# Kernel optimization log

Hardware: AMD Instinct MI355X
Metric: run time of the kernel (lower is better)

The kernel has to match this reference:

```python
import jax, jax.numpy as jnp
import numpy as np

N = 50000      # nodes
E = 800000     # edges (avg degree 16)
DIN = 128      # input_dim
DH = 128       # hidden_dim
H = 8          # num_heads
DK = DH // H   # 16
TN = 8         # num_node_types
TE = 8         # num_edge_types
NB = 4         # num_bases


def setup_inputs() -> dict:
    key = jax.random.key(0)
    ks = jax.random.split(key, 20)
    inp = {}
    inp['node_feat'] = jax.random.normal(ks[0], (N, DIN), jnp.float32)
    inp['node_type'] = jax.random.randint(ks[1], (N,), 0, TN)
    inp['src'] = jax.random.randint(ks[2], (E,), 0, N)
    inp['dst'] = jax.random.randint(ks[3], (E,), 0, N)
    inp['edge_type'] = jax.random.randint(ks[4], (E,), 0, TE)
    s = 0.05
    for i, nm in enumerate(['k', 'q', 'v', 'a']):
        inp['w_comp_' + nm] = jax.random.normal(ks[5 + 2 * i], (TN, NB), jnp.float32) * s
        inp['w_basis_' + nm] = jax.random.normal(ks[6 + 2 * i], (NB, DIN * DH), jnp.float32) * s
    inp['relation_pri'] = jnp.ones((TE, H), jnp.float32)
    inp['relation_att'] = jax.random.uniform(ks[13], (TE, H, DK, DK), jnp.float32, -0.25, 0.25)
    inp['relation_msg'] = jax.random.uniform(ks[14], (TE, H, DK, DK), jnp.float32, -0.25, 0.25)
    inp['loop_weight'] = jax.random.uniform(ks[15], (DIN, DH), jnp.float32, -0.08, 0.08)
    inp['bias'] = jnp.zeros((DH,), jnp.float32)
    return inp


def _decomp(x, nt, w_comp, w_basis):
    # basis regularizer: per-node-type weight W[t] = sum_b w_comp[t,b] * basis[b]
    T = w_comp.shape[0]
    W = (w_comp @ w_basis).reshape(T, x.shape[-1], -1)   # [T, in, out]
    h_all = jnp.einsum('ni,tio->tno', x, W)              # [T, N, out]
    return h_all[nt, jnp.arange(x.shape[0])]             # gather per-node type


def reference(node_feat, node_type, src, dst, edge_type,
              w_comp_k, w_basis_k, w_comp_q, w_basis_q,
              w_comp_v, w_basis_v, w_comp_a, w_basis_a,
              relation_pri, relation_att, relation_msg, loop_weight, bias):
    n = node_feat.shape[0]
    scale = (DH / H) ** -0.5
    # node init: k/q/v projections (per-node-type basis transforms)
    k = _decomp(node_feat, node_type, w_comp_k, w_basis_k).reshape(n, H, DK)
    q = _decomp(node_feat, node_type, w_comp_q, w_basis_q).reshape(n, H, DK)
    v = _decomp(node_feat, node_type, w_comp_v, w_basis_v).reshape(n, H, DK)
    # edge init: HGT attention. kt = k[src] @ relation_att[etype], computed
    # per-type at node granularity then gathered (avoids [E,H,dk,dk] gather).
    kt = jnp.einsum('nhi,thij->tnhj', k, relation_att)[edge_type, src]   # [E,H,dk]
    e = (q[dst] * kt).sum(-1) * relation_pri[edge_type] * scale          # [E,H]
    # edge softmax over incoming edges of each dst node
    m = jax.ops.segment_max(e, dst, num_segments=n)
    ex = jnp.exp(e - m[dst])
    denom = jax.ops.segment_sum(ex, dst, num_segments=n)
    a = ex / denom[dst]                                                  # [E,H]
    # message: v[src] @ relation_msg[etype], weighted by attention, sum-reduce
    vt = jnp.einsum('nhi,thij->tnhj', v, relation_msg)[edge_type, src]   # [E,H,dk]
    agg = jax.ops.segment_sum(a[..., None] * vt, dst, num_segments=n)    # [N,H,dk]
    agg = agg.reshape(n, DH)
    # node update: a_transform + self loop + bias + relu (dropout=0, no BN)
    out = _decomp(agg, node_type, w_comp_a, w_basis_a)
    out = out + node_feat @ loop_weight + bias
    return jax.nn.relu(out)
```

## Files before the change

### kernel.cpp

```cpp
#include <hip/hip_runtime.h>
#include <hip/hip_bf16.h>
#include <stdint.h>

#define DIN 128
#define DHID 128
#define NHEAD 8
#define DKH 16
#define TN 8
#define TE 8
#define NBASE 4

typedef short s8v __attribute__((ext_vector_type(8)));
typedef float f4v __attribute__((ext_vector_type(4)));

static __device__ __forceinline__ float bf2f(__hip_bfloat16 x){ return __bfloat162float(x); }
static __device__ __forceinline__ float lo16f(uint32_t u){ return __builtin_bit_cast(float, u << 16); }
static __device__ __forceinline__ float hi16f(uint32_t u){ return __builtin_bit_cast(float, u & 0xFFFF0000u); }
static __device__ __forceinline__ uint16_t f2bfu(float x){ return __builtin_bit_cast(uint16_t, __float2bfloat16(x)); }
static __device__ __forceinline__ uint32_t packbf2(float lo, float hi){
    return (uint32_t)f2bfu(lo) | ((uint32_t)f2bfu(hi) << 16);
}
static __device__ __forceinline__ float ldf(const void* p, int i, int flag){
    return flag ? ((const float*)p)[i] : bf2f(((const __hip_bfloat16*)p)[i]);
}

__global__ void k_hist(const int* __restrict__ dst, int E,
                       const int* __restrict__ ntype, int Nn,
                       int* __restrict__ deg, int* __restrict__ tcount,
                       const uint32_t* __restrict__ rpri_raw, int* __restrict__ dflag)
{
    __shared__ int lt[TN];
    if (threadIdx.x < TN) lt[threadIdx.x] = 0;
    if (blockIdx.x == 0 && threadIdx.x == 0) {
        dflag[0] = (rpri_raw[0] == 0x3F803F80u) ? 0 : 1;
    }
    __syncthreads();
    int stride = gridDim.x * blockDim.x;
    int i0 = blockIdx.x * blockDim.x + threadIdx.x;
    for (int e = i0; e < E; e += stride) atomicAdd(&deg[dst[e]], 1);
    for (int n = i0; n < Nn; n += stride) atomicAdd(&lt[ntype[n]], 1);
    __syncthreads();
    if (threadIdx.x < TN) atomicAdd(&tcount[threadIdx.x], lt[threadIdx.x]);
}

__global__ void k_convert(const void* __restrict__ xin, uint32_t* __restrict__ xbf,
                          int nWords, const int* __restrict__ dflag)
{
    int flag = dflag[0];
    int i = blockIdx.x * 256 + threadIdx.x;
    int stride = gridDim.x * 256;
    if (flag) {
        const float2* f = (const float2*)xin;
        for (int w = i; w < nWords; w += stride) {
            float2 v = f[w];
            xbf[w] = packbf2(v.x, v.y);
        }
    } else {
        const uint32_t* s = (const uint32_t*)xin;
        for (int w = i; w < nWords; w += stride) xbf[w] = s[w];
    }
}

__global__ void k_weights(const void* __restrict__ ck, const void* __restrict__ bk,
                          const void* __restrict__ cq, const void* __restrict__ bq,
                          const void* __restrict__ cv, const void* __restrict__ bv,
                          const void* __restrict__ ca, const void* __restrict__ ba,
                          const void* __restrict__ lw,
                          __hip_bfloat16* __restrict__ WkqvT, __hip_bfloat16* __restrict__ WfinT,
                          const int* __restrict__ dflag)
{
    int flag = dflag[0];
    int idx = blockIdx.x * 256 + threadIdx.x;
    const int T1 = TN * 3 * 128 * 128;
    if (idx < T1) {
        int t = idx / 49152; int r = idx % 49152;
        int proj = r / 16384; int r2 = r % 16384;
        int j = r2 >> 7; int i = r2 & 127;
        const void* c = (proj == 0) ? ck : ((proj == 1) ? cq : cv);
        const void* b = (proj == 0) ? bk : ((proj == 1) ? bq : bv);
        float s = 0.f;
        #pragma unroll
        for (int bb = 0; bb < NBASE; ++bb)
            s += ldf(c, t * NBASE + bb, flag) * ldf(b, bb * 16384 + i * 128 + j, flag);
        WkqvT[idx] = __float2bfloat16(s);
    } else if (idx < T1 + TN * 128 * 256) {
        int r = idx - T1;
        int t = r >> 15; int r2 = r & 32767;
        int j = r2 >> 8; int kk = r2 & 255;
        float s;
        if (kk < 128) {
            s = 0.f;
            #pragma unroll
            for (int bb = 0; bb < NBASE; ++bb)
                s += ldf(ca, t * NBASE + bb, flag) * ldf(ba, bb * 16384 + kk * 128 + j, flag);
        } else {
            s = ldf(lw, (kk - 128) * 128 + j, flag);
        }
        WfinT[r] = __float2bfloat16(s);
    }
}

__global__ void __launch_bounds__(1024) k_scan(const int* __restrict__ deg,
                                               int* __restrict__ eoff, int* __restrict__ ecur,
                                               const int* __restrict__ tcount,
                                               int* __restrict__ toff, int* __restrict__ tcur, int Nn)
{
    __shared__ int wsum[16];
    __shared__ int carry_s;
    int tid = threadIdx.x, lane = tid & 63, wid = tid >> 6;
    if (tid == 0) carry_s = 0;
    __syncthreads();
    for (int base = 0; base < Nn; base += 4096) {
        int i0 = base + tid * 4;
        int v0 = (i0     < Nn) ? deg[i0]     : 0;
        int v1 = (i0 + 1 < Nn) ? deg[i0 + 1] : 0;
        int v2 = (i0 + 2 < Nn) ? deg[i0 + 2] : 0;
        int v3 = (i0 + 3 < Nn) ? deg[i0 + 3] : 0;
        int s = v0 + v1 + v2 + v3;
        int sc = s;
        #pragma unroll
        for (int off = 1; off < 64; off <<= 1) {
            int tt = __shfl_up(sc, off, 64);
            if (lane >= off) sc += tt;
        }
        if (lane == 63) wsum[wid] = sc;
        int carry = carry_s;
        __syncthreads();
        int wb = 0;
        for (int w = 0; w < wid; ++w) wb += wsum[w];
        int run = carry + wb + (sc - s);
        if (i0     < Nn) { eoff[i0]     = run; ecur[i0]     = run; } run += v0;
        if (i0 + 1 < Nn) { eoff[i0 + 1] = run; ecur[i0 + 1] = run; } run += v1;
        if (i0 + 2 < Nn) { eoff[i0 + 2] = run; ecur[i0 + 2] = run; } run += v2;
        if (i0 + 3 < Nn) { eoff[i0 + 3] = run; ecur[i0 + 3] = run; }
        __syncthreads();
        if (tid == 0) {
            int tot = 0;
            for (int w = 0; w < 16; ++w) tot += wsum[w];
            carry_s += tot;
        }
        __syncthreads();
    }
    if (tid == 0) {
        eoff[Nn] = carry_s;
        int s = 0;
        for (int t = 0; t < TN; ++t) { toff[t] = s; tcur[t] = s; s += tcount[t]; }
        toff[TN] = s;
    }
}

__global__ void k_scatter(const int* __restrict__ src, const int* __restrict__ dst,
                          const int* __restrict__ et, int E,
                          const int* __restrict__ ntype, int Nn,
                          int* __restrict__ ecur, int* __restrict__ esrc, int* __restrict__ eet,
                          int* __restrict__ tcur, int* __restrict__ perm)
{
    int stride = gridDim.x * blockDim.x;
    int i0 = blockIdx.x * blockDim.x + threadIdx.x;
    for (int e = i0; e < E; e += stride) {
        int p = atomicAdd(&ecur[dst[e]], 1);
        esrc[p] = src[e]; eet[p] = et[e];
    }
    for (int n = i0; n < Nn; n += stride) {
        int p = atomicAdd(&tcur[ntype[n]], 1);
        perm[p] = n;
    }
}

__global__ void __launch_bounds__(256, 1) k_proj(
    const __hip_bfloat16* __restrict__ xbf,
    const __hip_bfloat16* __restrict__ WkqvT,
    const int* __restrict__ perm, const int* __restrict__ ntype,
    __hip_bfloat16* __restrict__ k16, __hip_bfloat16* __restrict__ q16,
    __hip_bfloat16* __restrict__ v16, int Nn)
{
    int lane = threadIdx.x & 63;
    int wave = blockIdx.x * 4 + (threadIdx.x >> 6);
    int row0 = wave * 16;
    if (row0 >= Nn) return;
    int col = lane & 15, quad = lane >> 4;
    int ar = row0 + col;
    int anode = perm[(ar < Nn) ? ar : (Nn - 1)];
    int tfirst = ntype[perm[row0]];
    int last_i = row0 + 15; if (last_i >= Nn) last_i = Nn - 1;
    int tlast = ntype[perm[last_i]];
    int onode[4], otype[4];
    #pragma unroll
    for (int r = 0; r < 4; ++r) {
        int oi = row0 + quad * 4 + r;
        bool v = (oi < Nn);
        onode[r] = perm[v ? oi : (Nn - 1)];
        otype[r] = v ? ntype[onode[r]] : -1;
    }
    const s8v* arow = (const s8v*)(xbf + (size_t)anode * DIN);
    for (int t = tfirst; t <= tlast; ++t) {
        f4v acc[24];
        #pragma unroll
        for (int nb = 0; nb < 24; ++nb) acc[nb] = (f4v){0.f, 0.f, 0.f, 0.f};
        const __hip_bfloat16* bbase = WkqvT + (size_t)t * 49152;
        #pragma unroll
        for (int kq = 0; kq < 4; ++kq) {
            s8v a = arow[kq * 4 + quad];
            #pragma unroll
            for (int nb = 0; nb < 24; ++nb) {
                int J = nb * 16 + col;
                s8v b = *((const s8v*)(bbase + (size_t)J * 128) + (kq * 4 + quad));
                acc[nb] = __builtin_amdgcn_mfma_f32_16x16x32_bf16(a, b, acc[nb], 0, 0, 0);
            }
        }
        #pragma unroll
        for (int nb = 0; nb < 24; ++nb) {
            int jj = ((nb * 16) & 127) + col;
            __hip_bfloat16* outp = (nb < 8) ? k16 : ((nb < 16) ? q16 : v16);
            #pragma unroll
            for (int r = 0; r < 4; ++r) {
                if (otype[r] == t) outp[(size_t)onode[r] * DHID + jj] = __float2bfloat16(acc[nb][r]);
            }
        }
    }
}

__global__ void __launch_bounds__(512, 4) k_edge(
    const __hip_bfloat16* __restrict__ k16, const __hip_bfloat16* __restrict__ q16,
    const __hip_bfloat16* __restrict__ v16,
    const void* __restrict__ ratt, const void* __restrict__ rmsg,
    const void* __restrict__ rpri,
    const int* __restrict__ eoff, const int* __restrict__ esrc, const int* __restrict__ eet,
    __hip_bfloat16* __restrict__ aggbf, int Nn, const int* __restrict__ dflag)
{
    __shared__ uint32_t Au[8192];
    __shared__ uint32_t Mu[8192];
    int flag = dflag[0];
    int tid = threadIdx.x;
    for (int d = tid; d < 4096; d += 512) {
        int et = d >> 9, ip = (d >> 6) & 7, hh = (d >> 3) & 7, xx = d & 7;
        int i0 = ip * 2, j0 = xx * 2;
        int bidx = ((et * 8 + hh) * 16 + i0) * 16 + j0;
        int o = ((et * 64 + ip * 8 + hh) * 8 + xx) * 2;
        float ps = ldf(rpri, et * 8 + hh, flag) * 0.25f;
        {
            float a00 = ldf(ratt, bidx, flag) * ps,      a10 = ldf(ratt, bidx + 16, flag) * ps;
            float a01 = ldf(ratt, bidx + 1, flag) * ps,  a11 = ldf(ratt, bidx + 17, flag) * ps;
            Au[o] = packbf2(a00, a10); Au[o + 1] = packbf2(a01, a11);
        }
        {
            float a00 = ldf(rmsg, bidx, flag),      a10 = ldf(rmsg, bidx + 16, flag);
            float a01 = ldf(rmsg, bidx + 1, flag),  a11 = ldf(rmsg, bidx + 17, flag);
            Mu[o] = packbf2(a00, a10); Mu[o + 1] = packbf2(a01, a11);
        }
    }
    __syncthreads();
    int lane = tid & 63;
    int h = lane >> 3, x = lane & 7;
    int wid = blockIdx.x * 8 + (tid >> 6);
    int nw = gridDim.x * 8;
    const uint32_t* kp = (const uint32_t*)k16;
    const uint32_t* qp = (const uint32_t*)q16;
    const uint32_t* vp = (const uint32_t*)v16;
    int lbase = h * 16 + x * 2;
    for (int n = wid; n < Nn; n += nw) {
        uint32_t qw = qp[n * 64 + lane];
        float q0 = lo16f(qw), q1 = hi16f(qw);
        float l = 0.f, a0 = 0.f, a1 = 0.f;
        int p0 = eoff[n], p1 = eoff[n + 1];
        for (int base = p0; base < p1; base += 64) {
            int myp = base + lane;
            int se = 0, te = 0;
            if (myp < p1) { se = esrc[myp]; te = eet[myp]; }
            int cnt = p1 - base; if (cnt > 64) cnt = 64;

            auto process = [&](int j) {
                int srcn = __shfl(se, j, 64);
                int et   = __shfl(te, j, 64);
                const uint4* kr = (const uint4*)(kp + (size_t)srcn * 64 + h * 8);
                uint4 ka = kr[0], kb = kr[1];
                const uint4* vr = (const uint4*)(vp + (size_t)srcn * 64 + h * 8);
                uint4 va = vr[0], vb = vr[1];
                int tb = et * 1024 + lbase;
                float u0 = 0.f, u1 = 0.f;
                {
                    uint32_t w0[8] = {ka.x, ka.y, ka.z, ka.w, kb.x, kb.y, kb.z, kb.w};
                    #pragma unroll
                    for (int ip = 0; ip < 8; ++ip) {
                        float k0 = lo16f(w0[ip]), k1 = hi16f(w0[ip]);
                        uint2 av = *(const uint2*)&Au[tb + ip * 128];
                        u0 = fmaf(k0, lo16f(av.x), u0); u0 = fmaf(k1, hi16f(av.x), u0);
                        u1 = fmaf(k0, lo16f(av.y), u1); u1 = fmaf(k1, hi16f(av.y), u1);
                    }
                }
                float pl = u0 * q0 + u1 * q1;
                pl += __shfl_xor(pl, 1, 64);
                pl += __shfl_xor(pl, 2, 64);
                pl += __shfl_xor(pl, 4, 64);
                float ex = __expf(pl);
                float t0 = 0.f, t1 = 0.f;
                {
                    uint32_t w1[8] = {va.x, va.y, va.z, va.w, vb.x, vb.y, vb.z, vb.w};
                    #pragma unroll
                    for (int ip = 0; ip < 8; ++ip) {
                        float v0 = lo16f(w1[ip]), v1 = hi16f(w1[ip]);
                        uint2 mv = *(const uint2*)&Mu[tb + ip * 128];
                        t0 = fmaf(v0, lo16f(mv.x), t0); t0 = fmaf(v1, hi16f(mv.x), t0);
                        t1 = fmaf(v0, lo16f(mv.y), t1); t1 = fmaf(v1, hi16f(mv.y), t1);
                    }
                }
                l += ex;
                a0 = fmaf(ex, t0, a0);
                a1 = fmaf(ex, t1, a1);
            };

            int j = 0;
            for (; j + 1 < cnt; j += 2) { process(j); process(j + 1); }
            if (j < cnt) process(j);
        }
        float inv = (l > 0.f) ? (1.f / l) : 0.f;
        ((uint32_t*)aggbf)[(size_t)n * 64 + lane] = packbf2(a0 * inv, a1 * inv);
    }
}

__global__ void __launch_bounds__(256, 1) k_final(
    const __hip_bfloat16* __restrict__ xbf,
    const __hip_bfloat16* __restrict__ aggbf,
    const __hip_bfloat16* __restrict__ WfinT,
    const void* __restrict__ bias,
    const int* __restrict__ perm, const int* __restrict__ ntype,
    void* __restrict__ outv, int Nn, const int* __restrict__ dflag)
{
    int flag = dflag[0];
    int lane = threadIdx.x & 63;
    int wave = blockIdx.x * 4 + (threadIdx.x >> 6);
    int row0 = wave * 16;
    if (row0 >= Nn) return;
    int col = lane & 15, quad = lane >> 4;
    int ar = row0 + col;
    int anode = perm[(ar < Nn) ? ar : (Nn - 1)];
    int tfirst = ntype[perm[row0]];
    int last_i = row0 + 15; if (last_i >= Nn) last_i = Nn - 1;
    int tlast = ntype[perm[last_i]];
    int onode[4], otype[4];
    #pragma unroll
    for (int r = 0; r < 4; ++r) {
        int oi = row0 + quad * 4 + r;
        bool v = (oi < Nn);
        onode[r] = perm[v ? oi : (Nn - 1)];
        otype[r] = v ? ntype[onode[r]] : -1;
    }
    const s8v* arow0 = (const s8v*)(aggbf + (size_t)anode * DHID);
    const s8v* arow1 = (const s8v*)(xbf + (size_t)anode * DIN);
    for (int t = tfirst; t <= tlast; ++t) {
        f4v acc[8];
        #pragma unroll
        for (int nb = 0; nb < 8; ++nb) acc[nb] = (f4v){0.f, 0.f, 0.f, 0.f};
        const __hip_bfloat16* bbase = WfinT + (size_t)t * 32768;
        #pragma unroll
        for (int kq = 0; kq < 8; ++kq) {
            s8v a = (kq < 4) ? arow0[kq * 4 + quad] : arow1[(kq - 4) * 4 + quad];
            #pragma unroll
            for (int nb = 0; nb < 8; ++nb) {
                int J = nb * 16 + col;
                s8v b = *((const s8v*)(bbase + (size_t)J * 256) + (kq * 4 + quad));
                acc[nb] = __builtin_amdgcn_mfma_f32_16x16x32_bf16(a, b, acc[nb], 0, 0, 0);
            }
        }
        #pragma unroll
        for (int nb = 0; nb < 8; ++nb) {
            int J = nb * 16 + col;
            float bj = ldf(bias, J, flag);
            #pragma unroll
            for (int r = 0; r < 4; ++r) {
                if (otype[r] == t) {
                    float val = fmaxf(acc[nb][r] + bj, 0.f);
                    size_t oi = (size_t)onode[r] * DHID + J;
                    if (flag) ((float*)outv)[oi] = val;
                    else ((__hip_bfloat16*)outv)[oi] = __float2bfloat16(val);
                }
            }
        }
    }
}

extern "C" void kernel_launch(void* const* d_in, const int* in_sizes, int n_in,
                              void* d_out, int out_size, void* d_ws, size_t ws_size,
                              hipStream_t stream)
{
    const void* xfeat = d_in[0];
    const int* ntype = (const int*)d_in[1];
    const int* srcv  = (const int*)d_in[2];
    const int* dstv  = (const int*)d_in[3];
    const int* etypv = (const int*)d_in[4];
    const void* ck = d_in[5];
    const void* bk = d_in[6];
    const void* cq = d_in[7];
    const void* bq = d_in[8];
    const void* cv = d_in[9];
    const void* bv = d_in[10];
    const void* ca = d_in[11];
    const void* ba = d_in[12];
    const void* rpri = d_in[13];
    const void* ratt = d_in[14];
    const void* rmsg = d_in[15];
    const void* lw   = d_in[16];
    const void* bias = d_in[17];
    int Nn = in_sizes[1];
    int E  = in_sizes[2];

    char* w = (char*)d_ws;
    size_t off = 0;
    auto alloc = [&](size_t b) -> char* {
        char* r = w + off;
        off = (off + b + 255) & ~(size_t)255;
        return r;
    };
    __hip_bfloat16* WkqvT = (__hip_bfloat16*)alloc((size_t)TN * 3 * 128 * 128 * 2);
    __hip_bfloat16* WfinT = (__hip_bfloat16*)alloc((size_t)TN * 256 * 128 * 2);
    __hip_bfloat16* xbf = (__hip_bfloat16*)alloc((size_t)Nn * 128 * 2);
    __hip_bfloat16* k16 = (__hip_bfloat16*)alloc((size_t)Nn * 128 * 2);
    __hip_bfloat16* q16 = (__hip_bfloat16*)alloc((size_t)Nn * 128 * 2);
    __hip_bfloat16* v16 = (__hip_bfloat16*)alloc((size_t)Nn * 128 * 2);
    __hip_bfloat16* aggbf = (__hip_bfloat16*)alloc((size_t)Nn * 128 * 2);
    int* deg    = (int*)alloc((size_t)(Nn + TN) * 4);
    int* tcount = deg + Nn;
    int* eoff   = (int*)alloc((size_t)(Nn + 1) * 4);
    int* ecur   = (int*)alloc((size_t)Nn * 4);
    int* toff   = (int*)alloc((TN + 1) * 4);
    int* tcur   = (int*)alloc(TN * 4);
    int* perm   = (int*)alloc((size_t)Nn * 4);
    int* esrc   = (int*)alloc((size_t)E * 4);
    int* eet    = (int*)alloc((size_t)E * 4);
    int* dflag  = (int*)alloc(4);

    hipMemsetAsync(deg, 0, (size_t)(Nn + TN) * 4, stream);
    k_hist<<<2048, 256, 0, stream>>>(dstv, E, ntype, Nn, deg, tcount,
                                     (const uint32_t*)rpri, dflag);
    k_weights<<<2560, 256, 0, stream>>>(ck, bk, cq, bq, cv, bv, ca, ba, lw, WkqvT, WfinT, dflag);
    k_convert<<<2048, 256, 0, stream>>>(xfeat, (uint32_t*)xbf, Nn * 64, dflag);
    k_scan<<<1, 1024, 0, stream>>>(deg, eoff, ecur, tcount, toff, tcur, Nn);
    k_scatter<<<2048, 256, 0, stream>>>(srcv, dstv, etypv, E, ntype, Nn, ecur, esrc, eet, tcur, perm);
    int tiles = (Nn + 15) / 16;
    int pblocks = (tiles + 3) / 4;
    k_proj<<<pblocks, 256, 0, stream>>>(xbf, WkqvT, perm, ntype, k16, q16, v16, Nn);
    k_edge<<<1024, 512, 0, stream>>>(k16, q16, v16, ratt, rmsg, rpri, eoff, esrc, eet,
                                     aggbf, Nn, dflag);
    k_final<<<pblocks, 256, 0, stream>>>(xbf, aggbf, WfinT, bias, perm, ntype,
                                         d_out, Nn, dflag);
}
```

Before: 869.0 us.

## Hoist relation transforms out of edge loop via per-type q·A and deferred msg matmul

```diff
diff --git a/kernel.cpp b/kernel.cpp
--- a/kernel.cpp
+++ b/kernel.cpp
@@ -232,89 +232,114 @@
     __shared__ uint32_t Mu[8192];
     int flag = dflag[0];
     int tid = threadIdx.x;
-    for (int d = tid; d < 4096; d += 512) {
-        int et = d >> 9, ip = (d >> 6) & 7, hh = (d >> 3) & 7, xx = d & 7;
-        int i0 = ip * 2, j0 = xx * 2;
-        int bidx = ((et * 8 + hh) * 16 + i0) * 16 + j0;
-        int o = ((et * 64 + ip * 8 + hh) * 8 + xx) * 2;
+    for (int d = tid; d < 8192; d += 512) {
+        int et = d >> 10, hh = (d >> 7) & 7, p = (d >> 4) & 7, j = d & 15;
+        int src_i = ((et * 8 + hh) * 16 + 2 * p) * 16 + j;
+        int widx = ((et * 8 + hh) << 7) + ((p ^ hh) << 4) + ((j + 4 * hh) & 15);
         float ps = ldf(rpri, et * 8 + hh, flag) * 0.25f;
-        {
-            float a00 = ldf(ratt, bidx, flag) * ps,      a10 = ldf(ratt, bidx + 16, flag) * ps;
-            float a01 = ldf(ratt, bidx + 1, flag) * ps,  a11 = ldf(ratt, bidx + 17, flag) * ps;
-            Au[o] = packbf2(a00, a10); Au[o + 1] = packbf2(a01, a11);
-        }
-        {
-            float a00 = ldf(rmsg, bidx, flag),      a10 = ldf(rmsg, bidx + 16, flag);
-            float a01 = ldf(rmsg, bidx + 1, flag),  a11 = ldf(rmsg, bidx + 17, flag);
-            Mu[o] = packbf2(a00, a10); Mu[o + 1] = packbf2(a01, a11);
-        }
+        Au[widx] = packbf2(ldf(ratt, src_i, flag) * ps, ldf(ratt, src_i + 16, flag) * ps);
+        Mu[widx] = packbf2(ldf(rmsg, src_i, flag),      ldf(rmsg, src_i + 16, flag));
     }
     __syncthreads();
     int lane = tid & 63;
     int h = lane >> 3, x = lane & 7;
+    int gbase = lane & 56;
     int wid = blockIdx.x * 8 + (tid >> 6);
     int nw = gridDim.x * 8;
     const uint32_t* kp = (const uint32_t*)k16;
     const uint32_t* qp = (const uint32_t*)q16;
     const uint32_t* vp = (const uint32_t*)v16;
-    int lbase = h * 16 + x * 2;
     for (int n = wid; n < Nn; n += nw) {
-        uint32_t qw = qp[n * 64 + lane];
-        float q0 = lo16f(qw), q1 = hi16f(qw);
-        float l = 0.f, a0 = 0.f, a1 = 0.f;
         int p0 = eoff[n], p1 = eoff[n + 1];
+        int deg = p1 - p0;
+        int myp = p0 + lane;
+        int se = (myp < p1) ? esrc[myp] : 0;
+        int te = (myp < p1) ? eet[myp] : 8;
+        int mask;
+        if (deg > 64) mask = 255;
+        else {
+            mask = 0;
+            #pragma unroll
+            for (int e = 0; e < 8; ++e) if (__any(te == e)) mask |= (1 << e);
+        }
+        float qf[16];
+        #pragma unroll
+        for (int m = 0; m < 8; ++m) {
+            uint32_t qw = qp[(size_t)n * 64 + h * 8 + ((m - 2 * h) & 7)];
+            qf[2 * m] = lo16f(qw); qf[2 * m + 1] = hi16f(qw);
+        }
+        float qA0[8], qA1[8];
+        #pragma unroll
+        for (int e = 0; e < 8; ++e) { qA0[e] = 0.f; qA1[e] = 0.f; }
+        #pragma unroll
+        for (int e = 0; e < 8; ++e) if (mask & (1 << e)) {
+            const uint4* ab = (const uint4*)&Au[((e * 8 + h) << 7) + ((x ^ h) << 4)];
+            #pragma unroll
+            for (int c = 0; c < 4; ++c) {
+                uint4 w = ab[c];
+                qA0[e] = fmaf(lo16f(w.x), qf[4 * c + 0], qA0[e]); qA1[e] = fmaf(hi16f(w.x), qf[4 * c + 0], qA1[e]);
+                qA0[e] = fmaf(lo16f(w.y), qf[4 * c + 1], qA0[e]); qA1[e] = fmaf(hi16f(w.y), qf[4 * c + 1], qA1[e]);
+                qA0[e] = fmaf(lo16f(w.z), qf[4 * c + 2], qA0[e]); qA1[e] = fmaf(hi16f(w.z), qf[4 * c + 2], qA1[e]);
+                qA0[e] = fmaf(lo16f(w.w), qf[4 * c + 3], qA0[e]); qA1[e] = fmaf(hi16f(w.w), qf[4 * c + 3], qA1[e]);
+            }
+        }
+        float l = 0.f;
+        float S0[8], S1[8];
+        #pragma unroll
+        for (int e = 0; e < 8; ++e) { S0[e] = 0.f; S1[e] = 0.f; }
         for (int base = p0; base < p1; base += 64) {
-            int myp = base + lane;
-            int se = 0, te = 0;
-            if (myp < p1) { se = esrc[myp]; te = eet[myp]; }
+            if (base > p0) {
+                myp = base + lane;
+                se = (myp < p1) ? esrc[myp] : 0;
+                te = (myp < p1) ? eet[myp] : 8;
+            }
             int cnt = p1 - base; if (cnt > 64) cnt = 64;
-
-            auto process = [&](int j) {
-                int srcn = __shfl(se, j, 64);
-                int et   = __shfl(te, j, 64);
-                const uint4* kr = (const uint4*)(kp + (size_t)srcn * 64 + h * 8);
-                uint4 ka = kr[0], kb = kr[1];
-                const uint4* vr = (const uint4*)(vp + (size_t)srcn * 64 + h * 8);
-                uint4 va = vr[0], vb = vr[1];
-                int tb = et * 1024 + lbase;
-                float u0 = 0.f, u1 = 0.f;
-                {
-                    uint32_t w0[8] = {ka.x, ka.y, ka.z, ka.w, kb.x, kb.y, kb.z, kb.w};
-                    #pragma unroll
-                    for (int ip = 0; ip < 8; ++ip) {
-                        float k0 = lo16f(w0[ip]), k1 = hi16f(w0[ip]);
-                        uint2 av = *(const uint2*)&Au[tb + ip * 128];
-                        u0 = fmaf(k0, lo16f(av.x), u0); u0 = fmaf(k1, hi16f(av.x), u0);
-                        u1 = fmaf(k0, lo16f(av.y), u1); u1 = fmaf(k1, hi16f(av.y), u1);
-                    }
+            int sn = __builtin_amdgcn_readfirstlane(__shfl(se, 0, 64));
+            int en = __builtin_amdgcn_readfirstlane(__shfl(te, 0, 64));
+            uint32_t kw = kp[(size_t)sn * 64 + lane];
+            uint32_t vw = vp[(size_t)sn * 64 + lane];
+            for (int j = 0; j < cnt; ++j) {
+                int et_c = en; uint32_t kc = kw, vc = vw;
+                if (j + 1 < cnt) {
+                    sn = __builtin_amdgcn_readfirstlane(__shfl(se, j + 1, 64));
+                    en = __builtin_amdgcn_readfirstlane(__shfl(te, j + 1, 64));
+                    kw = kp[(size_t)sn * 64 + lane];
+                    vw = vp[(size_t)sn * 64 + lane];
                 }
-                float pl = u0 * q0 + u1 * q1;
-                pl += __shfl_xor(pl, 1, 64);
-                pl += __shfl_xor(pl, 2, 64);
-                pl += __shfl_xor(pl, 4, 64);
-                float ex = __expf(pl);
-                float t0 = 0.f, t1 = 0.f;
-                {
-                    uint32_t w1[8] = {va.x, va.y, va.z, va.w, vb.x, vb.y, vb.z, vb.w};
-                    #pragma unroll
-                    for (int ip = 0; ip < 8; ++ip) {
-                        float v0 = lo16f(w1[ip]), v1 = hi16f(w1[ip]);
-                        uint2 mv = *(const uint2*)&Mu[tb + ip * 128];
-                        t0 = fmaf(v0, lo16f(mv.x), t0); t0 = fmaf(v1, hi16f(mv.x), t0);
-                        t1 = fmaf(v0, lo16f(mv.y), t1); t1 = fmaf(v1, hi16f(mv.y), t1);
-                    }
+                float k0 = lo16f(kc), k1 = hi16f(kc);
+                float ep = 0.f;
+                #pragma unroll
+                for (int e = 0; e < 8; ++e) if (et_c == e) ep = k0 * qA0[e] + k1 * qA1[e];
+                ep += __shfl_xor(ep, 1, 64);
+                ep += __shfl_xor(ep, 2, 64);
+                ep += __shfl_xor(ep, 4, 64);
+                float ex = __expf(ep);
+                l += ex;
+                float v0 = lo16f(vc), v1 = hi16f(vc);
+                #pragma unroll
+                for (int e = 0; e < 8; ++e) if (et_c == e) {
+                    S0[e] = fmaf(ex, v0, S0[e]);
+                    S1[e] = fmaf(ex, v1, S1[e]);
                 }
-                l += ex;
-                a0 = fmaf(ex, t0, a0);
-                a1 = fmaf(ex, t1, a1);
-            };
-
-            int j = 0;
-            for (; j + 1 < cnt; j += 2) { process(j); process(j + 1); }
-            if (j < cnt) process(j);
+            }
+        }
+        float T0 = 0.f, T1 = 0.f;
+        int jrot = (2 * x + 4 * h) & 15;
+        #pragma unroll
+        for (int e = 0; e < 8; ++e) if (mask & (1 << e)) {
+            float s0sel = S0[e], s1sel = S1[e];
+            int wbase = ((e * 8 + h) << 7) + jrot;
+            #pragma unroll
+            for (int p = 0; p < 8; ++p) {
+                float sp0 = __shfl(s0sel, gbase | p, 64);
+                float sp1 = __shfl(s1sel, gbase | p, 64);
+                uint2 mw = *(const uint2*)&Mu[wbase + ((p ^ h) << 4)];
+                T0 = fmaf(lo16f(mw.x), sp0, T0); T0 = fmaf(hi16f(mw.x), sp1, T0);
+                T1 = fmaf(lo16f(mw.y), sp0, T1); T1 = fmaf(hi16f(mw.y), sp1, T1);
+            }
         }
         float inv = (l > 0.f) ? (1.f / l) : 0.f;
-        ((uint32_t*)aggbf)[(size_t)n * 64 + lane] = packbf2(a0 * inv, a1 * inv);
+        ((uint32_t*)aggbf)[(size_t)n * 64 + lane] = packbf2(T0 * inv, T1 * inv);
     }
 }
 
@@ -439,8 +464,8 @@
     int tiles = (Nn + 15) / 16;
     int pblocks = (tiles + 3) / 4;
     k_proj<<<pblocks, 256, 0, stream>>>(xbf, WkqvT, perm, ntype, k16, q16, v16, Nn);
-    k_edge<<<1024, 512, 0, stream>>>(k16, q16, v16, ratt, rmsg, rpri, eoff, esrc, eet,
-                                     aggbf, Nn, dflag);
+    k_edge<<<512, 512, 0, stream>>>(k16, q16, v16, ratt, rmsg, rpri, eoff, esrc, eet,
+                                    aggbf, Nn, dflag);
     k_final<<<pblocks, 256, 0, stream>>>(xbf, aggbf, WfinT, bias, perm, ntype,
                                          d_out, Nn, dflag);
 }
```

New measurement: 789.7 us. 9.1% less time.
